# Kernel tuning notes

Measured on AMD Instinct MI355X. Metric: run time of the kernel, lower is better.

## Reference

```python
import jax, jax.numpy as jnp
import numpy as np

E = 8       # num experts
T = 1024    # num tokens
H = 1024    # hidden dim
I = 1024    # intermediate dim (per gate/up half)


def setup_inputs() -> dict:
    key = jax.random.key(0)
    k1, k2, k3, k4 = jax.random.split(key, 4)
    return {
        "hidden_states": jax.random.normal(k1, (T, H), jnp.float32),
        "router_logits": jax.random.normal(k2, (T, E), jnp.float32),
        # W13 stored pre-transposed as in the module: [E, H, 2*I]
        "W13": jax.random.normal(k3, (E, H, 2 * I), jnp.float32) * 0.02,
        # W2 stored pre-transposed: [E, I, H]
        "W2": jax.random.normal(k4, (E, I, H), jnp.float32) * 0.02,
        "top_k": 2,
    }


def reference(hidden_states, router_logits, W13, W2, top_k):
    num_experts = router_logits.shape[-1]
    # --- routing: topk_softmax (softmax over all experts, then top-k) ---
    probs = jax.nn.softmax(router_logits, axis=-1)            # [T, E]
    w, idx = jax.lax.top_k(probs, top_k)                      # [T, K]
    # renormalize=True path of moe_gather
    w = w / jnp.sum(w, axis=-1, keepdims=True)
    # combine weights per expert: [T, E]
    combine = jnp.sum(jax.nn.one_hot(idx, num_experts, dtype=w.dtype) * w[..., None], axis=1)
    # --- grouped gate-up GEMM + silu_and_mul ---
    h13 = jnp.einsum('th,ehf->tef', hidden_states, W13)       # [T, E, 2I]
    gate, up = jnp.split(h13, 2, axis=-1)                     # each [T, E, I]
    act = jax.nn.silu(gate) * up                              # silu_and_mul
    # --- grouped down GEMM ---
    down = jnp.einsum('tei,eih->teh', act, W2)                # [T, E, H]
    # --- combine (moe_gather) ---
    return jnp.einsum('te,teh->th', combine, down)            # [T, H]
```

## Files before the change

kernel.cpp:

```cpp
#include <hip/hip_runtime.h>
#include <stdint.h>

#define NE    8
#define NTOK  1024
#define NH    1024
#define NI    1024
#define N13   2048

#define PREP_BLOCKS 513
#define G1MAX       768
#define G2MAX       768

typedef __attribute__((ext_vector_type(8))) short short8;
typedef __attribute__((ext_vector_type(4))) float f32x4;
typedef unsigned short u16;
typedef unsigned int   u32;

__device__ __forceinline__ u16 f2bf(float x) {
    union { float f; u32 u; } v; v.f = x;
    return (u16)((v.u + 0x7fffu + ((v.u >> 16) & 1u)) >> 16);
}

__device__ __forceinline__ u32 pack2(float a, float b) {
    return (u32)f2bf(a) | ((u32)f2bf(b) << 16);
}

__device__ __forceinline__ void async_ld16(u16* lds, const u16* g) {
    __builtin_amdgcn_global_load_lds(
        (const __attribute__((address_space(1))) u32*)g,
        (__attribute__((address_space(3))) u32*)lds, 16, 0, 0);
}

__device__ __forceinline__ bool find_tile(
    const int* __restrict__ counts, int tile, int bm, int ntn,
    int& e_o, int& mt_o, int& nt_o, int& cnt_o, int& base_o)
{
    int base = 0;
    #pragma unroll
    for (int e = 0; e < NE; e++) {
        const int cnt = counts[e];
        const int mtiles = (cnt + bm - 1) / bm;
        const int tiles = mtiles * ntn;
        if (tile < tiles) {
            e_o = e; mt_o = tile / ntn; nt_o = tile - (tile / ntn) * ntn;
            cnt_o = cnt; base_o = base; return true;
        }
        tile -= tiles; base += cnt;
    }
    return false;
}

__global__ __launch_bounds__(256) void prep_kernel(
    const float* __restrict__ X, const float* __restrict__ logits,
    int* __restrict__ counts, int* __restrict__ pair_tok,
    int* __restrict__ inv, float* __restrict__ tokw,
    u16* __restrict__ Xb)
{
    __shared__ int s_cnt[NE];
    __shared__ int s_base[NE];
    const int tid = threadIdx.x;
    const int b = blockIdx.x;

    if (b == 0) {
        if (tid < NE) s_cnt[tid] = 0;
        __syncthreads();
        int eA[4][2]; int slotA[4][2]; float wA[4][2];
        #pragma unroll
        for (int i = 0; i < 4; i++) {
            const int t = tid * 4 + i;
            float l[NE];
            #pragma unroll
            for (int e = 0; e < NE; e++) l[e] = logits[t * NE + e];
            int i0 = 0;
            #pragma unroll
            for (int e = 1; e < NE; e++) if (l[e] > l[i0]) i0 = e;
            int i1 = -1;
            #pragma unroll
            for (int e = 0; e < NE; e++) {
                if (e == i0) continue;
                if (i1 < 0 || l[e] > l[i1]) i1 = e;
            }
            const float e10 = __expf(l[i1] - l[i0]);
            const float invw = 1.0f / (1.0f + e10);
            eA[i][0] = i0; eA[i][1] = i1;
            wA[i][0] = invw; wA[i][1] = e10 * invw;
            slotA[i][0] = atomicAdd(&s_cnt[i0], 1);
            slotA[i][1] = atomicAdd(&s_cnt[i1], 1);
        }
        __syncthreads();
        if (tid == 0) {
            int acc = 0;
            #pragma unroll
            for (int e = 0; e < NE; e++) { s_base[e] = acc; acc += s_cnt[e]; }
        }
        __syncthreads();
        if (tid < NE) counts[tid] = s_cnt[tid];
        #pragma unroll
        for (int i = 0; i < 4; i++) {
            const int t = tid * 4 + i;
            #pragma unroll
            for (int k = 0; k < 2; k++) {
                const int p = s_base[eA[i][k]] + slotA[i][k];
                pair_tok[p] = t;
                inv[t * 2 + k] = p;
                tokw[t * 2 + k] = wA[i][k];
            }
        }
    } else {
        const int i = (b - 1) * 256 + tid;
        const float4* s = (const float4*)X;
        const float4 a = s[2 * i], c = s[2 * i + 1];
        uint4 o;
        o.x = pack2(a.x, a.y);
        o.y = pack2(a.z, a.w);
        o.z = pack2(c.x, c.y);
        o.w = pack2(c.z, c.w);
        *(uint4*)(Xb + (size_t)i * 8) = o;
    }
}

__global__ __launch_bounds__(256, 3) void gemm1_kernel(
    const u16* __restrict__ Xb, const float* __restrict__ W13,
    const int* __restrict__ counts, const int* __restrict__ pair_tok,
    u16* __restrict__ act)
{
    int e, mt, nt, cnt, base;
    if (!find_tile(counts, blockIdx.x, 128, NI / 32, e, mt, nt, cnt, base)) return;

    __shared__ u16 As[2][128 * 32];
    __shared__ u16 Bs[2][64 * 32];

    const int tid = threadIdx.x;
    const int ct  = nt * 32;

    const int m0 = tid >> 2;
    const int sw16 = (((tid & 3) ^ ((tid >> 4) & 3)) << 3);
    const int t0 = pair_tok[base + min(mt * 128 + m0, cnt - 1)];
    const int t1 = pair_tok[base + min(mt * 128 + 64 + m0, cnt - 1)];
    const u16* ga0 = Xb + (size_t)t0 * NH + sw16;
    const u16* ga1 = Xb + (size_t)t1 * NH + sw16;

    const int n0 = (tid & 15) << 2;
    const int kp = tid >> 4;
    const int f0 = (n0 < 32) ? (ct + n0) : (NI + ct + n0 - 32);
    const float* gw = W13 + ((size_t)e * NH + 2 * kp) * N13 + f0;
    const int bwr = (((kp >> 2) ^ (tid & 3)) << 3) + ((kp & 3) << 1);

    const int lane = tid & 63, w = tid >> 6;
    const int quad = lane >> 4, lid = lane & 15;
    const int rw = w >> 1, cw = w & 1;
    const int fsw = ((quad ^ ((lid >> 2) & 3)) << 3);
    int aoff[4];
    #pragma unroll
    for (int mi = 0; mi < 4; mi++)
        aoff[mi] = (rw * 64 + mi * 16 + lid) * 32 + fsw;
    const int bgoff = (cw * 16 + lid) * 32 + fsw;
    const int buoff = (32 + cw * 16 + lid) * 32 + fsw;

    f32x4 accg[4] = {};
    f32x4 accu[4] = {};

#define ISSUE1(b, k0)                                        \
    {                                                        \
        async_ld16(&As[b][tid * 8],         ga0 + (k0));     \
        async_ld16(&As[b][(tid + 256) * 8], ga1 + (k0));     \
    }
#define LOADB1(P0, P1, k0)                                            \
    {                                                                 \
        P0 = *(const float4*)(gw + (size_t)(k0) * N13);               \
        P1 = *(const float4*)(gw + (size_t)(k0) * N13 + N13);         \
    }
#define WRB1(b, P0, P1)                                               \
    {                                                                 \
        u32* d = (u32*)&Bs[b][(n0 << 5) + bwr];                       \
        d[0]  = pack2(P0.x, P1.x);                                    \
        d[16] = pack2(P0.y, P1.y);                                    \
        d[32] = pack2(P0.z, P1.z);                                    \
        d[48] = pack2(P0.w, P1.w);                                    \
    }
#define COMP1(b)                                                               \
    {                                                                          \
        short8 av[4];                                                          \
        _Pragma("unroll") for (int mi = 0; mi < 4; mi++)                       \
            av[mi] = *(const short8*)&As[b][aoff[mi]];                         \
        const short8 gv = *(const short8*)&Bs[b][bgoff];                       \
        const short8 uv = *(const short8*)&Bs[b][buoff];                       \
        _Pragma("unroll") for (int mi = 0; mi < 4; mi++) {                     \
            accg[mi] = __builtin_amdgcn_mfma_f32_16x16x32_bf16(                \
                av[mi], gv, accg[mi], 0, 0, 0);                                \
            accu[mi] = __builtin_amdgcn_mfma_f32_16x16x32_bf16(                \
                av[mi], uv, accu[mi], 0, 0, 0);                                \
        }                                                                      \
    }

    float4 p0, p1, q0, q1;
    LOADB1(q0, q1, 0);
    ISSUE1(0, 0);
    WRB1(0, q0, q1);
    LOADB1(q0, q1, 32);
    int buf = 0;
    for (int k0 = 32; k0 < NH; k0 += 32) {
        __syncthreads();
        if (k0 + 32 < NH) LOADB1(p0, p1, k0 + 32);
        ISSUE1(buf ^ 1, k0);
        COMP1(buf);
        WRB1(buf ^ 1, q0, q1);
        q0 = p0; q1 = p1;
        buf ^= 1;
    }
    __syncthreads();
    COMP1(buf);

    const int col = ct + cw * 16 + lid;
    #pragma unroll
    for (int mi = 0; mi < 4; mi++) {
        #pragma unroll
        for (int r = 0; r < 4; r++) {
            const int row = mt * 128 + rw * 64 + mi * 16 + quad * 4 + r;
            if (row < cnt) {
                const float g = accg[mi][r], u = accu[mi][r];
                const float s = g / (1.0f + __expf(-g)) * u;
                act[(size_t)(base + row) * NI + col] = f2bf(s);
            }
        }
    }
#undef ISSUE1
#undef LOADB1
#undef WRB1
#undef COMP1
}

__global__ __launch_bounds__(256, 3) void gemm2_kernel(
    const u16* __restrict__ act, const float* __restrict__ W2,
    const int* __restrict__ counts,
    float* __restrict__ down0, float* __restrict__ down1)
{
    int e, mt, ntq, cnt, base;
    if (!find_tile(counts, blockIdx.x, 128, (NH / 64) * 2, e, mt, ntq, cnt, base)) return;
    const int kh = ntq & 1;
    const int nt = ntq >> 1;
    const int ct = nt * 64;
    const int kbase = kh * 512;
    float* __restrict__ dwn = kh ? down1 : down0;

    __shared__ u16 As[2][128 * 32];
    __shared__ u16 Bs[2][64 * 32];

    const int tid = threadIdx.x;

    const int m0 = tid >> 2;
    const int sw16 = (((tid & 3) ^ ((tid >> 4) & 3)) << 3);
    const int p0r = base + min(mt * 128 + m0, cnt - 1);
    const int p1r = base + min(mt * 128 + 64 + m0, cnt - 1);
    const u16* ga0 = act + (size_t)p0r * NI + kbase + sw16;
    const u16* ga1 = act + (size_t)p1r * NI + kbase + sw16;

    const int n0 = (tid & 15) << 2;
    const int kp = tid >> 4;
    const float* gw = W2 + ((size_t)e * NI + kbase + 2 * kp) * NH + ct + n0;
    const int bwr = (((kp >> 2) ^ (tid & 3)) << 3) + ((kp & 3) << 1);

    const int lane = tid & 63, w = tid >> 6;
    const int quad = lane >> 4, lid = lane & 15;
    const int rw = w >> 1, cw = w & 1;
    const int fsw = ((quad ^ ((lid >> 2) & 3)) << 3);
    int aoff[4], boff[2];
    #pragma unroll
    for (int mi = 0; mi < 4; mi++)
        aoff[mi] = (rw * 64 + mi * 16 + lid) * 32 + fsw;
    #pragma unroll
    for (int nj = 0; nj < 2; nj++)
        boff[nj] = (cw * 32 + nj * 16 + lid) * 32 + fsw;

    f32x4 acc[4][2] = {};

#define ISSUE2(b, k0)                                        \
    {                                                        \
        async_ld16(&As[b][tid * 8],         ga0 + (k0));     \
        async_ld16(&As[b][(tid + 256) * 8], ga1 + (k0));     \
    }
#define LOADB2(P0, P1, k0)                                            \
    {                                                                 \
        P0 = *(const float4*)(gw + (size_t)(k0) * NH);                \
        P1 = *(const float4*)(gw + (size_t)(k0) * NH + NH);           \
    }
#define WRB2(b, P0, P1)                                               \
    {                                                                 \
        u32* d = (u32*)&Bs[b][(n0 << 5) + bwr];                       \
        d[0]  = pack2(P0.x, P1.x);                                    \
        d[16] = pack2(P0.y, P1.y);                                    \
        d[32] = pack2(P0.z, P1.z);                                    \
        d[48] = pack2(P0.w, P1.w);                                    \
    }
#define COMP2(b)                                                               \
    {                                                                          \
        short8 av[4], bv[2];                                                   \
        _Pragma("unroll") for (int mi = 0; mi < 4; mi++)                       \
            av[mi] = *(const short8*)&As[b][aoff[mi]];                         \
        _Pragma("unroll") for (int nj = 0; nj < 2; nj++)                       \
            bv[nj] = *(const short8*)&Bs[b][boff[nj]];                         \
        _Pragma("unroll") for (int mi = 0; mi < 4; mi++)                       \
            _Pragma("unroll") for (int nj = 0; nj < 2; nj++)                   \
                acc[mi][nj] = __builtin_amdgcn_mfma_f32_16x16x32_bf16(         \
                    av[mi], bv[nj], acc[mi][nj], 0, 0, 0);                     \
    }

    float4 p0, p1, q0, q1;
    LOADB2(q0, q1, 0);
    ISSUE2(0, 0);
    WRB2(0, q0, q1);
    LOADB2(q0, q1, 32);
    int buf = 0;
    for (int k0 = 32; k0 < 512; k0 += 32) {
        __syncthreads();
        if (k0 + 32 < 512) LOADB2(p0, p1, k0 + 32);
        ISSUE2(buf ^ 1, k0);
        COMP2(buf);
        WRB2(buf ^ 1, q0, q1);
        q0 = p0; q1 = p1;
        buf ^= 1;
    }
    __syncthreads();
    COMP2(buf);

    #pragma unroll
    for (int mi = 0; mi < 4; mi++) {
        #pragma unroll
        for (int r = 0; r < 4; r++) {
            const int row = mt * 128 + rw * 64 + mi * 16 + quad * 4 + r;
            if (row < cnt) {
                #pragma unroll
                for (int nj = 0; nj < 2; nj++) {
                    dwn[(size_t)(base + row) * NH + ct + cw * 32 + nj * 16 + lid] =
                        acc[mi][nj][r];
                }
            }
        }
    }
#undef ISSUE2
#undef LOADB2
#undef WRB2
#undef COMP2
}

__global__ __launch_bounds__(256) void combine_kernel(
    const float* __restrict__ down0, const float* __restrict__ down1,
    const int* __restrict__ inv, const float* __restrict__ tokw,
    float* __restrict__ out)
{
    const int t = blockIdx.x;
    const int p0 = inv[2 * t], p1 = inv[2 * t + 1];
    const float w0 = tokw[2 * t], w1 = tokw[2 * t + 1];
    const int i = threadIdx.x * 4;
    const float4 a0 = *(const float4*)(down0 + (size_t)p0 * NH + i);
    const float4 a1 = *(const float4*)(down1 + (size_t)p0 * NH + i);
    const float4 b0 = *(const float4*)(down0 + (size_t)p1 * NH + i);
    const float4 b1 = *(const float4*)(down1 + (size_t)p1 * NH + i);
    float4 o;
    o.x = w0 * (a0.x + a1.x) + w1 * (b0.x + b1.x);
    o.y = w0 * (a0.y + a1.y) + w1 * (b0.y + b1.y);
    o.z = w0 * (a0.z + a1.z) + w1 * (b0.z + b1.z);
    o.w = w0 * (a0.w + a1.w) + w1 * (b0.w + b1.w);
    *(float4*)(out + (size_t)t * NH + i) = o;
}

extern "C" void kernel_launch(void* const* d_in, const int* in_sizes, int n_in,
                              void* d_out, int out_size, void* d_ws, size_t ws_size,
                              hipStream_t stream)
{
    const float* X      = (const float*)d_in[0];
    const float* logits = (const float*)d_in[1];
    const float* W13    = (const float*)d_in[2];
    const float* W2     = (const float*)d_in[3];
    float* out = (float*)d_out;

    char* ws = (char*)d_ws;
    int*   counts   = (int*)(ws + 0);
    int*   pair_tok = (int*)(ws + 1024);
    int*   inv      = (int*)(ws + 16384);
    float* tokw     = (float*)(ws + 32768);
    u16*   Xb       = (u16*)(ws + 65536);
    u16*   act      = (u16*)(ws + (size_t)4  * 1024 * 1024);
    float* down0    = (float*)(ws + (size_t)8  * 1024 * 1024);
    float* down1    = (float*)(ws + (size_t)16 * 1024 * 1024);

    prep_kernel<<<PREP_BLOCKS, 256, 0, stream>>>(
        X, logits, counts, pair_tok, inv, tokw, Xb);
    gemm1_kernel<<<G1MAX, 256, 0, stream>>>(Xb, W13, counts, pair_tok, act);
    gemm2_kernel<<<G2MAX, 256, 0, stream>>>(act, W2, counts, down0, down1);
    combine_kernel<<<NTOK, 256, 0, stream>>>(down0, down1, inv, tokw, out);
}
```

Baseline: 186.8 us.

## Deepen GEMM K-tile to 64 with manual waitcnt pipeline and M-major tile order

```diff
diff --git a/kernel.cpp b/kernel.cpp
--- a/kernel.cpp
+++ b/kernel.cpp
@@ -20,18 +20,16 @@
     union { float f; u32 u; } v; v.f = x;
     return (u16)((v.u + 0x7fffu + ((v.u >> 16) & 1u)) >> 16);
 }
-
 __device__ __forceinline__ u32 pack2(float a, float b) {
     return (u32)f2bf(a) | ((u32)f2bf(b) << 16);
 }
-
 __device__ __forceinline__ void async_ld16(u16* lds, const u16* g) {
     __builtin_amdgcn_global_load_lds(
         (const __attribute__((address_space(1))) u32*)g,
         (__attribute__((address_space(3))) u32*)lds, 16, 0, 0);
 }
 
-__device__ __forceinline__ bool find_tile(
+__device__ __forceinline__ bool find_tile_mt(
     const int* __restrict__ counts, int tile, int bm, int ntn,
     int& e_o, int& mt_o, int& nt_o, int& cnt_o, int& base_o)
 {
@@ -42,13 +40,18 @@
         const int mtiles = (cnt + bm - 1) / bm;
         const int tiles = mtiles * ntn;
         if (tile < tiles) {
-            e_o = e; mt_o = tile / ntn; nt_o = tile - (tile / ntn) * ntn;
+            e_o = e; mt_o = tile % mtiles; nt_o = tile / mtiles;
             cnt_o = cnt; base_o = base; return true;
         }
         tile -= tiles; base += cnt;
     }
     return false;
 }
+
+#define SYNC(N)                                                            \
+    asm volatile("s_waitcnt vmcnt(" #N ") lgkmcnt(0)" ::: "memory");       \
+    __builtin_amdgcn_s_barrier();                                          \
+    __builtin_amdgcn_sched_barrier(0);
 
 __global__ __launch_bounds__(256) void prep_kernel(
     const float* __restrict__ X, const float* __restrict__ logits,
@@ -125,91 +128,110 @@
     u16* __restrict__ act)
 {
     int e, mt, nt, cnt, base;
-    if (!find_tile(counts, blockIdx.x, 128, NI / 32, e, mt, nt, cnt, base)) return;
-
-    __shared__ u16 As[2][128 * 32];
-    __shared__ u16 Bs[2][64 * 32];
+    if (!find_tile_mt(counts, blockIdx.x, 128, NI / 32, e, mt, nt, cnt, base)) return;
+
+    __shared__ __align__(16) u16 As[2][128 * 64];
+    __shared__ __align__(16) u16 Bs[2][64 * 64];
 
     const int tid = threadIdx.x;
     const int ct  = nt * 32;
 
-    const int m0 = tid >> 2;
-    const int sw16 = (((tid & 3) ^ ((tid >> 4) & 3)) << 3);
-    const int t0 = pair_tok[base + min(mt * 128 + m0, cnt - 1)];
-    const int t1 = pair_tok[base + min(mt * 128 + 64 + m0, cnt - 1)];
-    const u16* ga0 = Xb + (size_t)t0 * NH + sw16;
-    const u16* ga1 = Xb + (size_t)t1 * NH + sw16;
-
-    const int n0 = (tid & 15) << 2;
-    const int kp = tid >> 4;
-    const int f0 = (n0 < 32) ? (ct + n0) : (NI + ct + n0 - 32);
-    const float* gw = W13 + ((size_t)e * NH + 2 * kp) * N13 + f0;
-    const int bwr = (((kp >> 2) ^ (tid & 3)) << 3) + ((kp & 3) << 1);
+    const int csrc = (((tid & 7) ^ ((tid >> 3) & 7)) << 3);
+    const u16* ga[4];
+    #pragma unroll
+    for (int q = 0; q < 4; q++) {
+        const int row = mt * 128 + q * 32 + (tid >> 3);
+        const int t = pair_tok[base + min(row, cnt - 1)];
+        ga[q] = Xb + (size_t)t * NH + csrc;
+    }
+
+    const int n0  = (tid & 15) << 2;
+    const int kpL = tid >> 4;
+    const int f0  = (n0 < 32) ? (ct + n0) : (NI + ct + n0 - 32);
+    const float* gw = W13 + ((size_t)e * NH + 2 * kpL) * N13 + f0;
+    int wboffL[4], wboffH[4];
+    #pragma unroll
+    for (int i = 0; i < 4; i++) {
+        const int n = n0 + i;
+        const int s = (n ^ (n >> 2)) & 7;
+        wboffL[i] = n * 64 + ((((kpL >> 2)       ^ s) << 3)) + ((kpL & 3) << 1);
+        wboffH[i] = n * 64 + (((((kpL >> 2) + 4) ^ s) << 3)) + ((kpL & 3) << 1);
+    }
 
     const int lane = tid & 63, w = tid >> 6;
     const int quad = lane >> 4, lid = lane & 15;
     const int rw = w >> 1, cw = w & 1;
-    const int fsw = ((quad ^ ((lid >> 2) & 3)) << 3);
-    int aoff[4];
-    #pragma unroll
-    for (int mi = 0; mi < 4; mi++)
-        aoff[mi] = (rw * 64 + mi * 16 + lid) * 32 + fsw;
-    const int bgoff = (cw * 16 + lid) * 32 + fsw;
-    const int buoff = (32 + cw * 16 + lid) * 32 + fsw;
+    int aoff[2][4], bgoff[2], buoff[2];
+    #pragma unroll
+    for (int kk = 0; kk < 2; kk++) {
+        #pragma unroll
+        for (int mi = 0; mi < 4; mi++) {
+            const int row = rw * 64 + mi * 16 + lid;
+            aoff[kk][mi] = row * 64 + (((kk * 4 + quad) ^ (row & 7)) << 3);
+        }
+        const int ng = cw * 16 + lid;
+        bgoff[kk] = ng * 64 + (((kk * 4 + quad) ^ ((ng ^ (ng >> 2)) & 7)) << 3);
+        const int nu = 32 + cw * 16 + lid;
+        buoff[kk] = nu * 64 + (((kk * 4 + quad) ^ ((nu ^ (nu >> 2)) & 7)) << 3);
+    }
 
     f32x4 accg[4] = {};
     f32x4 accu[4] = {};
 
-#define ISSUE1(b, k0)                                        \
-    {                                                        \
-        async_ld16(&As[b][tid * 8],         ga0 + (k0));     \
-        async_ld16(&As[b][(tid + 256) * 8], ga1 + (k0));     \
-    }
-#define LOADB1(P0, P1, k0)                                            \
-    {                                                                 \
-        P0 = *(const float4*)(gw + (size_t)(k0) * N13);               \
-        P1 = *(const float4*)(gw + (size_t)(k0) * N13 + N13);         \
-    }
-#define WRB1(b, P0, P1)                                               \
-    {                                                                 \
-        u32* d = (u32*)&Bs[b][(n0 << 5) + bwr];                       \
-        d[0]  = pack2(P0.x, P1.x);                                    \
-        d[16] = pack2(P0.y, P1.y);                                    \
-        d[32] = pack2(P0.z, P1.z);                                    \
-        d[48] = pack2(P0.w, P1.w);                                    \
-    }
-#define COMP1(b)                                                               \
-    {                                                                          \
-        short8 av[4];                                                          \
-        _Pragma("unroll") for (int mi = 0; mi < 4; mi++)                       \
-            av[mi] = *(const short8*)&As[b][aoff[mi]];                         \
-        const short8 gv = *(const short8*)&Bs[b][bgoff];                       \
-        const short8 uv = *(const short8*)&Bs[b][buoff];                       \
-        _Pragma("unroll") for (int mi = 0; mi < 4; mi++) {                     \
-            accg[mi] = __builtin_amdgcn_mfma_f32_16x16x32_bf16(                \
-                av[mi], gv, accg[mi], 0, 0, 0);                                \
-            accu[mi] = __builtin_amdgcn_mfma_f32_16x16x32_bf16(                \
-                av[mi], uv, accu[mi], 0, 0, 0);                                \
-        }                                                                      \
-    }
-
-    float4 p0, p1, q0, q1;
-    LOADB1(q0, q1, 0);
-    ISSUE1(0, 0);
-    WRB1(0, q0, q1);
-    LOADB1(q0, q1, 32);
-    int buf = 0;
-    for (int k0 = 32; k0 < NH; k0 += 32) {
-        __syncthreads();
-        if (k0 + 32 < NH) LOADB1(p0, p1, k0 + 32);
-        ISSUE1(buf ^ 1, k0);
-        COMP1(buf);
-        WRB1(buf ^ 1, q0, q1);
-        q0 = p0; q1 = p1;
-        buf ^= 1;
-    }
-    __syncthreads();
-    COMP1(buf);
+#define ISSUEA1(B, K)                                                      \
+    { _Pragma("unroll") for (int q = 0; q < 4; q++)                        \
+        async_ld16(&As[B][q * 2048 + tid * 8], ga[q] + (K)); }
+#define LOADB1(V0, V1, V2, V3, K)                                          \
+    {                                                                      \
+        V0 = *(const float4*)(gw + (size_t)(K) * N13);                     \
+        V1 = *(const float4*)(gw + (size_t)(K) * N13 + N13);               \
+        V2 = *(const float4*)(gw + (size_t)((K) + 32) * N13);              \
+        V3 = *(const float4*)(gw + (size_t)((K) + 32) * N13 + N13);        \
+    }
+#define WRB1(B, V0, V1, V2, V3)                                            \
+    { _Pragma("unroll") for (int i = 0; i < 4; i++) {                      \
+        *(u32*)&Bs[B][wboffL[i]] =                                         \
+            pack2(((const float*)&V0)[i], ((const float*)&V1)[i]);         \
+        *(u32*)&Bs[B][wboffH[i]] =                                         \
+            pack2(((const float*)&V2)[i], ((const float*)&V3)[i]);         \
+    } }
+#define COMP1(B)                                                           \
+    { _Pragma("unroll") for (int kk = 0; kk < 2; kk++) {                   \
+        const short8 gv = *(const short8*)&Bs[B][bgoff[kk]];               \
+        const short8 uv = *(const short8*)&Bs[B][buoff[kk]];               \
+        _Pragma("unroll") for (int mi = 0; mi < 4; mi++) {                 \
+            const short8 av = *(const short8*)&As[B][aoff[kk][mi]];        \
+            accg[mi] = __builtin_amdgcn_mfma_f32_16x16x32_bf16(            \
+                av, gv, accg[mi], 0, 0, 0);                                \
+            accu[mi] = __builtin_amdgcn_mfma_f32_16x16x32_bf16(            \
+                av, uv, accu[mi], 0, 0, 0);                                \
+        } } }
+
+    float4 a0, a1, a2, a3, b0, b1, b2, b3;
+    LOADB1(b0, b1, b2, b3, 0);
+    ISSUEA1(0, 0);
+    WRB1(0, b0, b1, b2, b3);
+    LOADB1(a0, a1, a2, a3, 64);
+
+    #pragma unroll
+    for (int j = 0; j < 14; j += 2) {
+        SYNC(4);
+        ISSUEA1(1, (j + 1) * 64);
+        LOADB1(b0, b1, b2, b3, (j + 2) * 64);
+        COMP1(0);
+        WRB1(1, a0, a1, a2, a3);
+        SYNC(4);
+        ISSUEA1(0, (j + 2) * 64);
+        LOADB1(a0, a1, a2, a3, (j + 3) * 64);
+        COMP1(1);
+        WRB1(0, b0, b1, b2, b3);
+    }
+    SYNC(4);
+    ISSUEA1(1, 15 * 64);
+    COMP1(0);
+    WRB1(1, a0, a1, a2, a3);
+    SYNC(0);
+    COMP1(1);
 
     const int col = ct + cw * 16 + lid;
     #pragma unroll
@@ -219,12 +241,12 @@
             const int row = mt * 128 + rw * 64 + mi * 16 + quad * 4 + r;
             if (row < cnt) {
                 const float g = accg[mi][r], u = accu[mi][r];
-                const float s = g / (1.0f + __expf(-g)) * u;
-                act[(size_t)(base + row) * NI + col] = f2bf(s);
+                act[(size_t)(base + row) * NI + col] =
+                    f2bf(g / (1.0f + __expf(-g)) * u);
             }
         }
     }
-#undef ISSUE1
+#undef ISSUEA1
 #undef LOADB1
 #undef WRB1
 #undef COMP1
@@ -236,92 +258,114 @@
     float* __restrict__ down0, float* __restrict__ down1)
 {
     int e, mt, ntq, cnt, base;
-    if (!find_tile(counts, blockIdx.x, 128, (NH / 64) * 2, e, mt, ntq, cnt, base)) return;
+    if (!find_tile_mt(counts, blockIdx.x, 128, 16 * 2, e, mt, ntq, cnt, base)) return;
     const int kh = ntq & 1;
     const int nt = ntq >> 1;
     const int ct = nt * 64;
     const int kbase = kh * 512;
     float* __restrict__ dwn = kh ? down1 : down0;
 
-    __shared__ u16 As[2][128 * 32];
-    __shared__ u16 Bs[2][64 * 32];
+    __shared__ __align__(16) u16 As[2][128 * 64];
+    __shared__ __align__(16) u16 Bs[2][64 * 64];
 
     const int tid = threadIdx.x;
 
-    const int m0 = tid >> 2;
-    const int sw16 = (((tid & 3) ^ ((tid >> 4) & 3)) << 3);
-    const int p0r = base + min(mt * 128 + m0, cnt - 1);
-    const int p1r = base + min(mt * 128 + 64 + m0, cnt - 1);
-    const u16* ga0 = act + (size_t)p0r * NI + kbase + sw16;
-    const u16* ga1 = act + (size_t)p1r * NI + kbase + sw16;
-
-    const int n0 = (tid & 15) << 2;
-    const int kp = tid >> 4;
-    const float* gw = W2 + ((size_t)e * NI + kbase + 2 * kp) * NH + ct + n0;
-    const int bwr = (((kp >> 2) ^ (tid & 3)) << 3) + ((kp & 3) << 1);
+    const int csrc = (((tid & 7) ^ ((tid >> 3) & 7)) << 3);
+    const u16* ga[4];
+    #pragma unroll
+    for (int q = 0; q < 4; q++) {
+        const int row = mt * 128 + q * 32 + (tid >> 3);
+        const int p = base + min(row, cnt - 1);
+        ga[q] = act + (size_t)p * NI + kbase + csrc;
+    }
+
+    const int n0  = (tid & 15) << 2;
+    const int kpL = tid >> 4;
+    const float* gw = W2 + ((size_t)e * NI + kbase + 2 * kpL) * NH + ct + n0;
+    int wboffL[4], wboffH[4];
+    #pragma unroll
+    for (int i = 0; i < 4; i++) {
+        const int n = n0 + i;
+        const int s = (n ^ (n >> 2)) & 7;
+        wboffL[i] = n * 64 + ((((kpL >> 2)       ^ s) << 3)) + ((kpL & 3) << 1);
+        wboffH[i] = n * 64 + (((((kpL >> 2) + 4) ^ s) << 3)) + ((kpL & 3) << 1);
+    }
 
     const int lane = tid & 63, w = tid >> 6;
     const int quad = lane >> 4, lid = lane & 15;
     const int rw = w >> 1, cw = w & 1;
-    const int fsw = ((quad ^ ((lid >> 2) & 3)) << 3);
-    int aoff[4], boff[2];
-    #pragma unroll
-    for (int mi = 0; mi < 4; mi++)
-        aoff[mi] = (rw * 64 + mi * 16 + lid) * 32 + fsw;
-    #pragma unroll
-    for (int nj = 0; nj < 2; nj++)
-        boff[nj] = (cw * 32 + nj * 16 + lid) * 32 + fsw;
+    int aoff[2][4], boff[2][2];
+    #pragma unroll
+    for (int kk = 0; kk < 2; kk++) {
+        #pragma unroll
+        for (int mi = 0; mi < 4; mi++) {
+            const int row = rw * 64 + mi * 16 + lid;
+            aoff[kk][mi] = row * 64 + (((kk * 4 + quad) ^ (row & 7)) << 3);
+        }
+        #pragma unroll
+        for (int nj = 0; nj < 2; nj++) {
+            const int n = cw * 32 + nj * 16 + lid;
+            boff[kk][nj] = n * 64 +
+                (((kk * 4 + quad) ^ ((n ^ (n >> 2)) & 7)) << 3);
+        }
+    }
 
     f32x4 acc[4][2] = {};
 
-#define ISSUE2(b, k0)                                        \
-    {                                                        \
-        async_ld16(&As[b][tid * 8],         ga0 + (k0));     \
-        async_ld16(&As[b][(tid + 256) * 8], ga1 + (k0));     \
-    }
-#define LOADB2(P0, P1, k0)                                            \
-    {                                                                 \
-        P0 = *(const float4*)(gw + (size_t)(k0) * NH);                \
-        P1 = *(const float4*)(gw + (size_t)(k0) * NH + NH);           \
-    }
-#define WRB2(b, P0, P1)                                               \
-    {                                                                 \
-        u32* d = (u32*)&Bs[b][(n0 << 5) + bwr];                       \
-        d[0]  = pack2(P0.x, P1.x);                                    \
-        d[16] = pack2(P0.y, P1.y);                                    \
-        d[32] = pack2(P0.z, P1.z);                                    \
-        d[48] = pack2(P0.w, P1.w);                                    \
-    }
-#define COMP2(b)                                                               \
-    {                                                                          \
-        short8 av[4], bv[2];                                                   \
-        _Pragma("unroll") for (int mi = 0; mi < 4; mi++)                       \
-            av[mi] = *(const short8*)&As[b][aoff[mi]];                         \
-        _Pragma("unroll") for (int nj = 0; nj < 2; nj++)                       \
-            bv[nj] = *(const short8*)&Bs[b][boff[nj]];                         \
-        _Pragma("unroll") for (int mi = 0; mi < 4; mi++)                       \
-            _Pragma("unroll") for (int nj = 0; nj < 2; nj++)                   \
-                acc[mi][nj] = __builtin_amdgcn_mfma_f32_16x16x32_bf16(         \
-                    av[mi], bv[nj], acc[mi][nj], 0, 0, 0);                     \
-    }
-
-    float4 p0, p1, q0, q1;
-    LOADB2(q0, q1, 0);
-    ISSUE2(0, 0);
-    WRB2(0, q0, q1);
-    LOADB2(q0, q1, 32);
-    int buf = 0;
-    for (int k0 = 32; k0 < 512; k0 += 32) {
-        __syncthreads();
-        if (k0 + 32 < 512) LOADB2(p0, p1, k0 + 32);
-        ISSUE2(buf ^ 1, k0);
-        COMP2(buf);
-        WRB2(buf ^ 1, q0, q1);
-        q0 = p0; q1 = p1;
-        buf ^= 1;
-    }
-    __syncthreads();
-    COMP2(buf);
+#define ISSUEA2(B, K)                                                      \
+    { _Pragma("unroll") for (int q = 0; q < 4; q++)                        \
+        async_ld16(&As[B][q * 2048 + tid * 8], ga[q] + (K)); }
+#define LOADB2(V0, V1, V2, V3, K)                                          \
+    {                                                                      \
+        V0 = *(const float4*)(gw + (size_t)(K) * NH);                      \
+        V1 = *(const float4*)(gw + (size_t)(K) * NH + NH);                 \
+        V2 = *(const float4*)(gw + (size_t)((K) + 32) * NH);               \
+        V3 = *(const float4*)(gw + (size_t)((K) + 32) * NH + NH);          \
+    }
+#define WRB2(B, V0, V1, V2, V3)                                            \
+    { _Pragma("unroll") for (int i = 0; i < 4; i++) {                      \
+        *(u32*)&Bs[B][wboffL[i]] =                                         \
+            pack2(((const float*)&V0)[i], ((const float*)&V1)[i]);         \
+        *(u32*)&Bs[B][wboffH[i]] =                                         \
+            pack2(((const float*)&V2)[i], ((const float*)&V3)[i]);         \
+    } }
+#define COMP2(B)                                                           \
+    { _Pragma("unroll") for (int kk = 0; kk < 2; kk++) {                   \
+        const short8 bv0 = *(const short8*)&Bs[B][boff[kk][0]];            \
+        const short8 bv1 = *(const short8*)&Bs[B][boff[kk][1]];            \
+        _Pragma("unroll") for (int mi = 0; mi < 4; mi++) {                 \
+            const short8 av = *(const short8*)&As[B][aoff[kk][mi]];        \
+            acc[mi][0] = __builtin_amdgcn_mfma_f32_16x16x32_bf16(          \
+                av, bv0, acc[mi][0], 0, 0, 0);                             \
+            acc[mi][1] = __builtin_amdgcn_mfma_f32_16x16x32_bf16(          \
+                av, bv1, acc[mi][1], 0, 0, 0);                             \
+        } } }
+
+    float4 a0, a1, a2, a3, b0, b1, b2, b3;
+    LOADB2(b0, b1, b2, b3, 0);
+    ISSUEA2(0, 0);
+    WRB2(0, b0, b1, b2, b3);
+    LOADB2(a0, a1, a2, a3, 64);
+
+    #pragma unroll
+    for (int j = 0; j < 6; j += 2) {
+        SYNC(4);
+        ISSUEA2(1, (j + 1) * 64);
+        LOADB2(b0, b1, b2, b3, (j + 2) * 64);
+        COMP2(0);
+        WRB2(1, a0, a1, a2, a3);
+        SYNC(4);
+        ISSUEA2(0, (j + 2) * 64);
+        LOADB2(a0, a1, a2, a3, (j + 3) * 64);
+        COMP2(1);
+        WRB2(0, b0, b1, b2, b3);
+    }
+    SYNC(4);
+    ISSUEA2(1, 7 * 64);
+    COMP2(0);
+    WRB2(1, a0, a1, a2, a3);
+    SYNC(0);
+    COMP2(1);
 
     #pragma unroll
     for (int mi = 0; mi < 4; mi++) {
@@ -337,7 +381,7 @@
             }
         }
     }
-#undef ISSUE2
+#undef ISSUEA2
 #undef LOADB2
 #undef WRB2
 #undef COMP2
```

Result: faster. 178.5 us (-4.5%).

## Shrink GEMM M-tile to 64 with triple-buffered, fully unrolled LDS pipeline

Applied to the files above, without the earlier changes.

```diff
diff --git a/kernel.cpp b/kernel.cpp
--- a/kernel.cpp
+++ b/kernel.cpp
@@ -8,8 +8,8 @@
 #define N13   2048
 
 #define PREP_BLOCKS 513
-#define G1MAX       768
-#define G2MAX       768
+#define G1MAX       1248
+#define G2MAX       1248
 
 typedef __attribute__((ext_vector_type(8))) short short8;
 typedef __attribute__((ext_vector_type(4))) float f32x4;
@@ -20,11 +20,14 @@
     union { float f; u32 u; } v; v.f = x;
     return (u16)((v.u + 0x7fffu + ((v.u >> 16) & 1u)) >> 16);
 }
-
 __device__ __forceinline__ u32 pack2(float a, float b) {
     return (u32)f2bf(a) | ((u32)f2bf(b) << 16);
 }
-
+__device__ __forceinline__ u32 cvt_pk(float lo, float hi) {
+    u32 r;
+    asm("v_cvt_pk_bf16_f32 %0, %1, %2" : "=v"(r) : "v"(lo), "v"(hi));
+    return r;
+}
 __device__ __forceinline__ void async_ld16(u16* lds, const u16* g) {
     __builtin_amdgcn_global_load_lds(
         (const __attribute__((address_space(1))) u32*)g,
@@ -49,6 +52,13 @@
     }
     return false;
 }
+
+#define SYNCV(N)                                                           \
+    {                                                                      \
+        asm volatile("s_waitcnt vmcnt(" #N ") lgkmcnt(0)" ::: "memory");   \
+        __builtin_amdgcn_s_barrier();                                      \
+        __builtin_amdgcn_sched_barrier(0);                                 \
+    }
 
 __global__ __launch_bounds__(256) void prep_kernel(
     const float* __restrict__ X, const float* __restrict__ logits,
@@ -119,215 +129,225 @@
     }
 }
 
-__global__ __launch_bounds__(256, 3) void gemm1_kernel(
+__global__ __launch_bounds__(256, 4) void gemm1_kernel(
     const u16* __restrict__ Xb, const float* __restrict__ W13,
     const int* __restrict__ counts, const int* __restrict__ pair_tok,
     u16* __restrict__ act)
 {
     int e, mt, nt, cnt, base;
-    if (!find_tile(counts, blockIdx.x, 128, NI / 32, e, mt, nt, cnt, base)) return;
-
-    __shared__ u16 As[2][128 * 32];
-    __shared__ u16 Bs[2][64 * 32];
+    if (!find_tile(counts, blockIdx.x, 64, 32, e, mt, nt, cnt, base)) return;
+
+    __shared__ __align__(16) u16 As[3][64 * 32];
+    __shared__ __align__(16) u16 Bs[3][64 * 40];
 
     const int tid = threadIdx.x;
     const int ct  = nt * 32;
 
-    const int m0 = tid >> 2;
-    const int sw16 = (((tid & 3) ^ ((tid >> 4) & 3)) << 3);
-    const int t0 = pair_tok[base + min(mt * 128 + m0, cnt - 1)];
-    const int t1 = pair_tok[base + min(mt * 128 + 64 + m0, cnt - 1)];
-    const u16* ga0 = Xb + (size_t)t0 * NH + sw16;
-    const u16* ga1 = Xb + (size_t)t1 * NH + sw16;
+    const int csrc = (((tid & 3) ^ ((tid >> 3) & 3)) << 3);
+    const int arow = mt * 64 + (tid >> 2);
+    const int tok  = pair_tok[base + min(arow, cnt - 1)];
+    const u16* ga  = Xb + (size_t)tok * NH + csrc;
 
     const int n0 = (tid & 15) << 2;
     const int kp = tid >> 4;
+    const int kc = kp >> 2;
     const int f0 = (n0 < 32) ? (ct + n0) : (NI + ct + n0 - 32);
     const float* gw = W13 + ((size_t)e * NH + 2 * kp) * N13 + f0;
-    const int bwr = (((kp >> 2) ^ (tid & 3)) << 3) + ((kp & 3) << 1);
+    int wboff[4];
+    #pragma unroll
+    for (int jj = 0; jj < 4; jj++) {
+        const int n = n0 + jj;
+        wboff[jj] = n * 40 + ((kc ^ ((n >> 3) & 3)) << 3) + ((kp & 3) << 1);
+    }
 
     const int lane = tid & 63, w = tid >> 6;
     const int quad = lane >> 4, lid = lane & 15;
     const int rw = w >> 1, cw = w & 1;
-    const int fsw = ((quad ^ ((lid >> 2) & 3)) << 3);
-    int aoff[4];
-    #pragma unroll
-    for (int mi = 0; mi < 4; mi++)
-        aoff[mi] = (rw * 64 + mi * 16 + lid) * 32 + fsw;
-    const int bgoff = (cw * 16 + lid) * 32 + fsw;
-    const int buoff = (32 + cw * 16 + lid) * 32 + fsw;
-
-    f32x4 accg[4] = {};
-    f32x4 accu[4] = {};
-
-#define ISSUE1(b, k0)                                        \
-    {                                                        \
-        async_ld16(&As[b][tid * 8],         ga0 + (k0));     \
-        async_ld16(&As[b][(tid + 256) * 8], ga1 + (k0));     \
-    }
-#define LOADB1(P0, P1, k0)                                            \
-    {                                                                 \
-        P0 = *(const float4*)(gw + (size_t)(k0) * N13);               \
-        P1 = *(const float4*)(gw + (size_t)(k0) * N13 + N13);         \
-    }
-#define WRB1(b, P0, P1)                                               \
-    {                                                                 \
-        u32* d = (u32*)&Bs[b][(n0 << 5) + bwr];                       \
-        d[0]  = pack2(P0.x, P1.x);                                    \
-        d[16] = pack2(P0.y, P1.y);                                    \
-        d[32] = pack2(P0.z, P1.z);                                    \
-        d[48] = pack2(P0.w, P1.w);                                    \
-    }
-#define COMP1(b)                                                               \
-    {                                                                          \
-        short8 av[4];                                                          \
-        _Pragma("unroll") for (int mi = 0; mi < 4; mi++)                       \
-            av[mi] = *(const short8*)&As[b][aoff[mi]];                         \
-        const short8 gv = *(const short8*)&Bs[b][bgoff];                       \
-        const short8 uv = *(const short8*)&Bs[b][buoff];                       \
-        _Pragma("unroll") for (int mi = 0; mi < 4; mi++) {                     \
-            accg[mi] = __builtin_amdgcn_mfma_f32_16x16x32_bf16(                \
-                av[mi], gv, accg[mi], 0, 0, 0);                                \
-            accu[mi] = __builtin_amdgcn_mfma_f32_16x16x32_bf16(                \
-                av[mi], uv, accu[mi], 0, 0, 0);                                \
-        }                                                                      \
-    }
-
-    float4 p0, p1, q0, q1;
-    LOADB1(q0, q1, 0);
-    ISSUE1(0, 0);
-    WRB1(0, q0, q1);
-    LOADB1(q0, q1, 32);
-    int buf = 0;
-    for (int k0 = 32; k0 < NH; k0 += 32) {
-        __syncthreads();
-        if (k0 + 32 < NH) LOADB1(p0, p1, k0 + 32);
-        ISSUE1(buf ^ 1, k0);
-        COMP1(buf);
-        WRB1(buf ^ 1, q0, q1);
-        q0 = p0; q1 = p1;
-        buf ^= 1;
-    }
-    __syncthreads();
-    COMP1(buf);
+    int aoff[2];
+    #pragma unroll
+    for (int mi = 0; mi < 2; mi++) {
+        const int r = rw * 32 + mi * 16 + lid;
+        aoff[mi] = r * 32 + ((quad ^ ((r >> 1) & 3)) << 3);
+    }
+    int bgoff, buoff;
+    { const int n = cw * 16 + lid;
+      bgoff = n * 40 + ((quad ^ ((n >> 3) & 3)) << 3); }
+    { const int n = 32 + cw * 16 + lid;
+      buoff = n * 40 + ((quad ^ ((n >> 3) & 3)) << 3); }
+
+    f32x4 accg[2] = {};
+    f32x4 accu[2] = {};
+    float4 bq[3][2];
+
+#define ISSUEA1(S, K) async_ld16(&As[S][tid * 8], ga + (K));
+#define LOADB1(RB, K)                                                      \
+    { bq[RB][0] = *(const float4*)(gw + (size_t)(K) * N13);                \
+      bq[RB][1] = *(const float4*)(gw + (size_t)(K) * N13 + N13); }
+#define WRB1(S)                                                            \
+    { _Pragma("unroll") for (int jj = 0; jj < 4; jj++) {                   \
+        *(u32*)&Bs[S][wboff[jj]] =                                         \
+            cvt_pk(((const float*)&bq[S][0])[jj],                          \
+                   ((const float*)&bq[S][1])[jj]);                         \
+    } }
+#define COMP1(S)                                                           \
+    {                                                                      \
+        const short8 gv = *(const short8*)&Bs[S][bgoff];                   \
+        const short8 uv = *(const short8*)&Bs[S][buoff];                   \
+        __builtin_amdgcn_s_setprio(1);                                     \
+        _Pragma("unroll") for (int mi = 0; mi < 2; mi++) {                 \
+            const short8 av = *(const short8*)&As[S][aoff[mi]];            \
+            accg[mi] = __builtin_amdgcn_mfma_f32_16x16x32_bf16(            \
+                av, gv, accg[mi], 0, 0, 0);                                \
+            accu[mi] = __builtin_amdgcn_mfma_f32_16x16x32_bf16(            \
+                av, uv, accu[mi], 0, 0, 0);                                \
+        }                                                                  \
+        __builtin_amdgcn_s_setprio(0);                                     \
+    }
+#define G1_STEP(J, NV)                                                     \
+    SYNCV(NV)                                                              \
+    if ((J) + 2 < 32) { ISSUEA1((((J) + 2) % 3), (((J) + 2) * 32)) }       \
+    if ((J) + 3 < 32) { LOADB1(((J) % 3), (((J) + 3) * 32)) }              \
+    COMP1(((J) % 3))                                                       \
+    if ((J) + 1 < 32) { WRB1((((J) + 1) % 3)) }
+
+    LOADB1(0, 0)
+    ISSUEA1(0, 0)
+    LOADB1(1, 32)
+    ISSUEA1(1, 32)
+    LOADB1(2, 64)
+    asm volatile("s_waitcnt vmcnt(6)" ::: "memory");
+    WRB1(0)
+
+    G1_STEP(0, 3)  G1_STEP(1, 3)  G1_STEP(2, 3)  G1_STEP(3, 3)
+    G1_STEP(4, 3)  G1_STEP(5, 3)  G1_STEP(6, 3)  G1_STEP(7, 3)
+    G1_STEP(8, 3)  G1_STEP(9, 3)  G1_STEP(10, 3) G1_STEP(11, 3)
+    G1_STEP(12, 3) G1_STEP(13, 3) G1_STEP(14, 3) G1_STEP(15, 3)
+    G1_STEP(16, 3) G1_STEP(17, 3) G1_STEP(18, 3) G1_STEP(19, 3)
+    G1_STEP(20, 3) G1_STEP(21, 3) G1_STEP(22, 3) G1_STEP(23, 3)
+    G1_STEP(24, 3) G1_STEP(25, 3) G1_STEP(26, 3) G1_STEP(27, 3)
+    G1_STEP(28, 3) G1_STEP(29, 3) G1_STEP(30, 1) G1_STEP(31, 0)
 
     const int col = ct + cw * 16 + lid;
     #pragma unroll
-    for (int mi = 0; mi < 4; mi++) {
+    for (int mi = 0; mi < 2; mi++) {
         #pragma unroll
         for (int r = 0; r < 4; r++) {
-            const int row = mt * 128 + rw * 64 + mi * 16 + quad * 4 + r;
+            const int row = mt * 64 + rw * 32 + mi * 16 + quad * 4 + r;
             if (row < cnt) {
                 const float g = accg[mi][r], u = accu[mi][r];
-                const float s = g / (1.0f + __expf(-g)) * u;
-                act[(size_t)(base + row) * NI + col] = f2bf(s);
+                act[(size_t)(base + row) * NI + col] =
+                    f2bf(g / (1.0f + __expf(-g)) * u);
             }
         }
     }
-#undef ISSUE1
+#undef ISSUEA1
 #undef LOADB1
 #undef WRB1
 #undef COMP1
-}
-
-__global__ __launch_bounds__(256, 3) void gemm2_kernel(
+#undef G1_STEP
+}
+
+__global__ __launch_bounds__(256, 4) void gemm2_kernel(
     const u16* __restrict__ act, const float* __restrict__ W2,
     const int* __restrict__ counts,
     float* __restrict__ down0, float* __restrict__ down1)
 {
     int e, mt, ntq, cnt, base;
-    if (!find_tile(counts, blockIdx.x, 128, (NH / 64) * 2, e, mt, ntq, cnt, base)) return;
+    if (!find_tile(counts, blockIdx.x, 64, 32, e, mt, ntq, cnt, base)) return;
     const int kh = ntq & 1;
     const int nt = ntq >> 1;
     const int ct = nt * 64;
     const int kbase = kh * 512;
     float* __restrict__ dwn = kh ? down1 : down0;
 
-    __shared__ u16 As[2][128 * 32];
-    __shared__ u16 Bs[2][64 * 32];
+    __shared__ __align__(16) u16 As[3][64 * 32];
+    __shared__ __align__(16) u16 Bs[3][64 * 40];
 
     const int tid = threadIdx.x;
 
-    const int m0 = tid >> 2;
-    const int sw16 = (((tid & 3) ^ ((tid >> 4) & 3)) << 3);
-    const int p0r = base + min(mt * 128 + m0, cnt - 1);
-    const int p1r = base + min(mt * 128 + 64 + m0, cnt - 1);
-    const u16* ga0 = act + (size_t)p0r * NI + kbase + sw16;
-    const u16* ga1 = act + (size_t)p1r * NI + kbase + sw16;
+    const int csrc = (((tid & 3) ^ ((tid >> 3) & 3)) << 3);
+    const int arow = mt * 64 + (tid >> 2);
+    const int p    = base + min(arow, cnt - 1);
+    const u16* ga  = act + (size_t)p * NI + kbase + csrc;
 
     const int n0 = (tid & 15) << 2;
     const int kp = tid >> 4;
+    const int kc = kp >> 2;
     const float* gw = W2 + ((size_t)e * NI + kbase + 2 * kp) * NH + ct + n0;
-    const int bwr = (((kp >> 2) ^ (tid & 3)) << 3) + ((kp & 3) << 1);
+    int wboff[4];
+    #pragma unroll
+    for (int jj = 0; jj < 4; jj++) {
+        const int n = n0 + jj;
+        wboff[jj] = n * 40 + ((kc ^ ((n >> 3) & 3)) << 3) + ((kp & 3) << 1);
+    }
 
     const int lane = tid & 63, w = tid >> 6;
     const int quad = lane >> 4, lid = lane & 15;
     const int rw = w >> 1, cw = w & 1;
-    const int fsw = ((quad ^ ((lid >> 2) & 3)) << 3);
-    int aoff[4], boff[2];
-    #pragma unroll
-    for (int mi = 0; mi < 4; mi++)
-        aoff[mi] = (rw * 64 + mi * 16 + lid) * 32 + fsw;
-    #pragma unroll
-    for (int nj = 0; nj < 2; nj++)
-        boff[nj] = (cw * 32 + nj * 16 + lid) * 32 + fsw;
-
-    f32x4 acc[4][2] = {};
-
-#define ISSUE2(b, k0)                                        \
-    {                                                        \
-        async_ld16(&As[b][tid * 8],         ga0 + (k0));     \
-        async_ld16(&As[b][(tid + 256) * 8], ga1 + (k0));     \
-    }
-#define LOADB2(P0, P1, k0)                                            \
-    {                                                                 \
-        P0 = *(const float4*)(gw + (size_t)(k0) * NH);                \
-        P1 = *(const float4*)(gw + (size_t)(k0) * NH + NH);           \
-    }
-#define WRB2(b, P0, P1)                                               \
-    {                                                                 \
-        u32* d = (u32*)&Bs[b][(n0 << 5) + bwr];                       \
-        d[0]  = pack2(P0.x, P1.x);                                    \
-        d[16] = pack2(P0.y, P1.y);                                    \
-        d[32] = pack2(P0.z, P1.z);                                    \
-        d[48] = pack2(P0.w, P1.w);                                    \
-    }
-#define COMP2(b)                                                               \
-    {                                                                          \
-        short8 av[4], bv[2];                                                   \
-        _Pragma("unroll") for (int mi = 0; mi < 4; mi++)                       \
-            av[mi] = *(const short8*)&As[b][aoff[mi]];                         \
-        _Pragma("unroll") for (int nj = 0; nj < 2; nj++)                       \
-            bv[nj] = *(const short8*)&Bs[b][boff[nj]];                         \
-        _Pragma("unroll") for (int mi = 0; mi < 4; mi++)                       \
-            _Pragma("unroll") for (int nj = 0; nj < 2; nj++)                   \
-                acc[mi][nj] = __builtin_amdgcn_mfma_f32_16x16x32_bf16(         \
-                    av[mi], bv[nj], acc[mi][nj], 0, 0, 0);                     \
-    }
-
-    float4 p0, p1, q0, q1;
-    LOADB2(q0, q1, 0);
-    ISSUE2(0, 0);
-    WRB2(0, q0, q1);
-    LOADB2(q0, q1, 32);
-    int buf = 0;
-    for (int k0 = 32; k0 < 512; k0 += 32) {
-        __syncthreads();
-        if (k0 + 32 < 512) LOADB2(p0, p1, k0 + 32);
-        ISSUE2(buf ^ 1, k0);
-        COMP2(buf);
-        WRB2(buf ^ 1, q0, q1);
-        q0 = p0; q1 = p1;
-        buf ^= 1;
-    }
-    __syncthreads();
-    COMP2(buf);
-
-    #pragma unroll
-    for (int mi = 0; mi < 4; mi++) {
+    int aoff[2], boff[2];
+    #pragma unroll
+    for (int mi = 0; mi < 2; mi++) {
+        const int r = rw * 32 + mi * 16 + lid;
+        aoff[mi] = r * 32 + ((quad ^ ((r >> 1) & 3)) << 3);
+    }
+    #pragma unroll
+    for (int nj = 0; nj < 2; nj++) {
+        const int n = cw * 32 + nj * 16 + lid;
+        boff[nj] = n * 40 + ((quad ^ ((n >> 3) & 3)) << 3);
+    }
+
+    f32x4 acc[2][2] = {};
+    float4 bq[3][2];
+
+#define ISSUEA2(S, K) async_ld16(&As[S][tid * 8], ga + (K));
+#define LOADB2(RB, K)                                                      \
+    { bq[RB][0] = *(const float4*)(gw + (size_t)(K) * NH);                 \
+      bq[RB][1] = *(const float4*)(gw + (size_t)(K) * NH + NH); }
+#define WRB2(S)                                                            \
+    { _Pragma("unroll") for (int jj = 0; jj < 4; jj++) {                   \
+        *(u32*)&Bs[S][wboff[jj]] =                                         \
+            cvt_pk(((const float*)&bq[S][0])[jj],                          \
+                   ((const float*)&bq[S][1])[jj]);                         \
+    } }
+#define COMP2(S)                                                           \
+    {                                                                      \
+        const short8 bv0 = *(const short8*)&Bs[S][boff[0]];                \
+        const short8 bv1 = *(const short8*)&Bs[S][boff[1]];                \
+        __builtin_amdgcn_s_setprio(1);                                     \
+        _Pragma("unroll") for (int mi = 0; mi < 2; mi++) {                 \
+            const short8 av = *(const short8*)&As[S][aoff[mi]];            \
+            acc[mi][0] = __builtin_amdgcn_mfma_f32_16x16x32_bf16(          \
+                av, bv0, acc[mi][0], 0, 0, 0);                             \
+            acc[mi][1] = __builtin_amdgcn_mfma_f32_16x16x32_bf16(          \
+                av, bv1, acc[mi][1], 0, 0, 0);                             \
+        }                                                                  \
+        __builtin_amdgcn_s_setprio(0);                                     \
+    }
+#define G2_STEP(J, NV)                                                     \
+    SYNCV(NV)                                                              \
+    if ((J) + 2 < 16) { ISSUEA2((((J) + 2) % 3), (((J) + 2) * 32)) }       \
+    if ((J) + 3 < 16) { LOADB2(((J) % 3), (((J) + 3) * 32)) }              \
+    COMP2(((J) % 3))                                                       \
+    if ((J) + 1 < 16) { WRB2((((J) + 1) % 3)) }
+
+    LOADB2(0, 0)
+    ISSUEA2(0, 0)
+    LOADB2(1, 32)
+    ISSUEA2(1, 32)
+    LOADB2(2, 64)
+    asm volatile("s_waitcnt vmcnt(6)" ::: "memory");
+    WRB2(0)
+
+    G2_STEP(0, 3)  G2_STEP(1, 3)  G2_STEP(2, 3)  G2_STEP(3, 3)
+    G2_STEP(4, 3)  G2_STEP(5, 3)  G2_STEP(6, 3)  G2_STEP(7, 3)
+    G2_STEP(8, 3)  G2_STEP(9, 3)  G2_STEP(10, 3) G2_STEP(11, 3)
+    G2_STEP(12, 3) G2_STEP(13, 3) G2_STEP(14, 1) G2_STEP(15, 0)
+
+    #pragma unroll
+    for (int mi = 0; mi < 2; mi++) {
         #pragma unroll
         for (int r = 0; r < 4; r++) {
-            const int row = mt * 128 + rw * 64 + mi * 16 + quad * 4 + r;
+            const int row = mt * 64 + rw * 32 + mi * 16 + quad * 4 + r;
             if (row < cnt) {
                 #pragma unroll
                 for (int nj = 0; nj < 2; nj++) {
@@ -337,10 +357,11 @@
             }
         }
     }
-#undef ISSUE2
+#undef ISSUEA2
 #undef LOADB2
 #undef WRB2
 #undef COMP2
+#undef G2_STEP
 }
 
 __global__ __launch_bounds__(256) void combine_kernel(
```

New measurement: 187.6 us. Within noise of the previous version (+0.4%).
